# Optimization experiments

Measured on AMD Instinct MI355X. Metric: run time of the kernel, lower is better.

The kernel has to match this reference:

```python
import jax, jax.numpy as jnp
import numpy as np

KS_LIST = (7, 9, 11)
DILS = (1, 2, 4, 8, 16, 32)
PER = 5          # kernels per (kernel_size, dilation) group
EPS = 1e-5       # BatchNorm1d eps
N, C, L = 512, 12, 8192


def _rocket_features(x, W7, b7, W9, b9, W11, b11):
    # x: [N, C, L]; W_ks: [6*PER, C, ks]; b_ks: [6*PER]
    dn = ('NCH', 'OIH', 'NCH')
    feats = []
    for W, b in ((W7, b7), (W9, b9), (W11, b11)):
        for j, d in enumerate(DILS):
            w = W[j * PER:(j + 1) * PER]      # [PER, C, ks]
            bb = b[j * PER:(j + 1) * PER]     # [PER]
            # one dilated conv for all PER kernels in this group -> [N, PER, L]
            out = jax.lax.conv_general_dilated(
                x, w, window_strides=(1,), padding='SAME',
                rhs_dilation=(d,), dimension_numbers=dn) + bb[None, :, None]
            ppv = jnp.mean((out > 0).astype(x.dtype), axis=2)  # [N, PER]
            mx = jnp.max(out, axis=2)                          # [N, PER]
            # interleave (ppv_k, max_k) per kernel, matching the torch loop order
            feats.append(jnp.stack([ppv, mx], axis=-1).reshape(x.shape[0], 2 * PER))
    f = jnp.concatenate(feats, axis=1)  # [N, 2*nb_kernels] = [N, 180]
    # BatchNorm1d(affine=False), training mode: batch stats, biased variance
    mean = jnp.mean(f, axis=0)
    var = jnp.var(f, axis=0)
    return (f - mean) / jnp.sqrt(var + EPS)


def setup_inputs() -> dict:
    key = jax.random.key(0)
    kx, k1, k2, k3, k4, k5, k6 = jax.random.split(key, 7)
    G = len(DILS) * PER  # 30 kernels per kernel-size family
    inp = {
        'x': jax.random.normal(kx, (N, C, L), dtype=jnp.float32),
        'W7': jax.random.uniform(k1, (G, C, 7), minval=-1.0, maxval=1.0, dtype=jnp.float32),
        'b7': jax.random.normal(k2, (G,), dtype=jnp.float32),
        'W9': jax.random.uniform(k3, (G, C, 9), minval=-1.0, maxval=1.0, dtype=jnp.float32),
        'b9': jax.random.normal(k4, (G,), dtype=jnp.float32),
        'W11': jax.random.uniform(k5, (G, C, 11), minval=-1.0, maxval=1.0, dtype=jnp.float32),
        'b11': jax.random.normal(k6, (G,), dtype=jnp.float32),
    }
    return inp


def reference(x, W7, b7, W9, b9, W11, b11):
    return _rocket_features(x, W7, b7, W9, b9, W11, b11)
```

## Files before the change

### kernel.cpp

```cpp
#include <hip/hip_runtime.h>
#include <math.h>
#include <limits.h>

#define N_SAMP 512
#define C_IN   12
#define L_IN   8192
#define NDIL   6
#define NFILT  30
#define NFEAT  180
#define NCHUNK 4
#define CHUNK  (L_IN / NCHUNK)
#define EPSV   1e-5f

#define HALO   160
#define TLC    1024
#define LWC    (TLC + 2*HALO)
#define CELLS  (LWC + (LWC >> 4) + 1)
#define TILEB  (CELLS * 16)
#define NST    (CHUNK / TLC)

#define WF_OFF (3 * N_SAMP * NCHUNK * NFILT * 2)
#define WTAB_B (NDIL * 3 * 64 * 16)

typedef __attribute__((ext_vector_type(4))) int i32x4;

__device__ __forceinline__ int cellb(int r) {
    return (r + (r >> 4)) << 4;
}

__device__ __forceinline__ int imax(int a, int b) { return a > b ? a : b; }

__global__ __launch_bounds__(256)
void build_wb(const float* __restrict__ W7, const float* __restrict__ W9,
              const float* __restrict__ W11, const float* __restrict__ b7,
              const float* __restrict__ b9, const float* __restrict__ b11,
              signed char* __restrict__ wc, signed char* __restrict__ wd,
              float* __restrict__ bias_tab)
{
    const int t = blockIdx.x * 256 + threadIdx.x;
    if (t < NDIL * 3 * 64) {
        const int j    = t / 192;
        const int mf   = (t / 64) % 3;
        const int lane = t % 64;
        const int col  = lane & 15;
        const int q    = lane >> 4;
        const int tap  = mf * 4 + q;
#pragma unroll
        for (int e = 0; e < 16; ++e) {
            float v = 0.0f;
            if (col < 15 && tap <= 10 && e < 12) {
                const int toff = tap - 5;
                if (col < 5) {
                    if (toff >= -3 && toff <= 3)
                        v = W7[((j * 5 + col) * 12 + e) * 7 + toff + 3];
                } else if (col < 10) {
                    if (toff >= -4 && toff <= 4)
                        v = W9[((j * 5 + col - 5) * 12 + e) * 9 + toff + 4];
                } else {
                    v = W11[((j * 5 + col - 10) * 12 + e) * 11 + toff + 5];
                }
            }
            const int W  = __float2int_rn(v * 8192.0f);
            const int C8 = (W + 128) >> 8;
            const int D8 = W - (C8 << 8);
            wc[(size_t)t * 16 + e] = (signed char)C8;
            wd[(size_t)t * 16 + e] = (signed char)D8;
        }
    } else if (t < NDIL * 3 * 64 + 96) {
        const int i = t - NDIL * 3 * 64;
        const int j = i / 16, s = i % 16;
        float b = 0.0f;
        if (s < 5)       b = b7 [j * 5 + s];
        else if (s < 10) b = b9 [j * 5 + s - 5];
        else if (s < 15) b = b11[j * 5 + s - 10];
        bias_tab[j * 16 + s] = b;
    }
}

__global__ __launch_bounds__(256)
void rocket_conv_i8(const float* __restrict__ x,
                    const signed char* __restrict__ wc,
                    const signed char* __restrict__ wd,
                    const float* __restrict__ bias_tab,
                    float* __restrict__ ws)
{
    __shared__ __align__(16) signed char xq[2][TILEB];
    __shared__ int scnt[NDIL * 16];
    __shared__ int smx [NDIL * 16];

    const int ch  = blockIdx.x;
    const int n   = blockIdx.y;
    const int tid = threadIdx.x;
    const int lane = tid & 63, wv = tid >> 6;
    const int row_l = lane & 15, q = lane >> 4;
    const float* __restrict__ xrow = x + (size_t)n * C_IN * L_IN;
    const i32x4* __restrict__ wcv = (const i32x4*)wc;
    const i32x4* __restrict__ wdv = (const i32x4*)wd;

    if (tid < NDIL * 16) { scnt[tid] = 0; smx[tid] = INT_MIN; }

    const int c0 = ch * CHUNK;
#pragma unroll 1
    for (int st = 0; st < NST; ++st) {
        const int t0 = c0 + st * TLC;
        __syncthreads();
#pragma unroll 1
        for (int r = tid; r < LWC; r += 256) {
            const int g = t0 - HALO + r;
            int h[4] = {0, 0, 0, 0}, l[4] = {0, 0, 0, 0};
            if ((unsigned)g < (unsigned)L_IN) {
#pragma unroll
                for (int c = 0; c < 12; ++c) {
                    const float xv = xrow[c * L_IN + g];
                    const int X  = __float2int_rn(xv * 4096.0f);
                    const int A8 = (X + 128) >> 8;
                    const int B8 = X - (A8 << 8);
                    h[c >> 2] |= (A8 & 255) << ((c & 3) * 8);
                    l[c >> 2] |= (B8 & 255) << ((c & 3) * 8);
                }
            }
            const int cell = cellb(r);
            *(i32x4*)&xq[0][cell] = (i32x4){h[0], h[1], h[2], h[3]};
            *(i32x4*)&xq[1][cell] = (i32x4){l[0], l[1], l[2], l[3]};
        }
        __syncthreads();

#pragma unroll 1
        for (int j = 0; j < NDIL; ++j) {
            const int d = 1 << j;
            const i32x4 C0 = wcv[(j * 3 + 0) * 64 + lane];
            const i32x4 C1 = wcv[(j * 3 + 1) * 64 + lane];
            const i32x4 C2 = wcv[(j * 3 + 2) * 64 + lane];
            const i32x4 D0 = wdv[(j * 3 + 0) * 64 + lane];
            const i32x4 D1 = wdv[(j * 3 + 1) * 64 + lane];
            const i32x4 D2 = wdv[(j * 3 + 2) * 64 + lane];
            const float bj = bias_tab[j * 16 + row_l];
            const int tj = (int)floorf(bj * -33554432.0f);
            const int r0 = HALO + wv * 256 + row_l + (q - 5) * d;
            const int r1 = HALO + wv * 256 + row_l + (q - 1) * d;
            const int r2 = HALO + wv * 256 + row_l +
                           ((q == 3) ? 0 : (q + 3) * d);

            int cnt_i = 0, mx_i = INT_MIN;
#pragma unroll 4
            for (int t = 0; t < 16; ++t) {
                const int cell0 = cellb(r0 + 16 * t);
                const int cell1 = cellb(r1 + 16 * t);
                const int cell2 = cellb(r2 + 16 * t);
                i32x4 a0 = {0, 0, 0, 0};
                i32x4 a1 = {0, 0, 0, 0};
                i32x4 a2 = {0, 0, 0, 0};
                {
                    i32x4 ah = *(const i32x4*)&xq[0][cell0];
                    i32x4 al = *(const i32x4*)&xq[1][cell0];
                    a0 = __builtin_amdgcn_mfma_i32_16x16x64_i8(ah, C0, a0, 0, 0, 0);
                    a1 = __builtin_amdgcn_mfma_i32_16x16x64_i8(ah, D0, a1, 0, 0, 0);
                    a1 = __builtin_amdgcn_mfma_i32_16x16x64_i8(al, C0, a1, 0, 0, 0);
                    a2 = __builtin_amdgcn_mfma_i32_16x16x64_i8(al, D0, a2, 0, 0, 0);
                }
                {
                    i32x4 ah = *(const i32x4*)&xq[0][cell1];
                    i32x4 al = *(const i32x4*)&xq[1][cell1];
                    a0 = __builtin_amdgcn_mfma_i32_16x16x64_i8(ah, C1, a0, 0, 0, 0);
                    a1 = __builtin_amdgcn_mfma_i32_16x16x64_i8(ah, D1, a1, 0, 0, 0);
                    a1 = __builtin_amdgcn_mfma_i32_16x16x64_i8(al, C1, a1, 0, 0, 0);
                    a2 = __builtin_amdgcn_mfma_i32_16x16x64_i8(al, D1, a2, 0, 0, 0);
                }
                {
                    i32x4 ah = *(const i32x4*)&xq[0][cell2];
                    i32x4 al = *(const i32x4*)&xq[1][cell2];
                    a0 = __builtin_amdgcn_mfma_i32_16x16x64_i8(ah, C2, a0, 0, 0, 0);
                    a1 = __builtin_amdgcn_mfma_i32_16x16x64_i8(ah, D2, a1, 0, 0, 0);
                    a1 = __builtin_amdgcn_mfma_i32_16x16x64_i8(al, C2, a1, 0, 0, 0);
                    a2 = __builtin_amdgcn_mfma_i32_16x16x64_i8(al, D2, a2, 0, 0, 0);
                }
                const int v0 = ((a0[0] << 8) + a1[0] << 8) + a2[0];
                const int v1 = ((a0[1] << 8) + a1[1] << 8) + a2[1];
                const int v2 = ((a0[2] << 8) + a1[2] << 8) + a2[2];
                const int v3 = ((a0[3] << 8) + a1[3] << 8) + a2[3];
                cnt_i += (v0 > tj) + (v1 > tj) + (v2 > tj) + (v3 > tj);
                mx_i = imax(mx_i, imax(imax(v0, v1), imax(v2, v3)));
            }

            cnt_i += __shfl_xor(cnt_i, 16);
            cnt_i += __shfl_xor(cnt_i, 32);
            mx_i = imax(mx_i, __shfl_xor(mx_i, 16));
            mx_i = imax(mx_i, __shfl_xor(mx_i, 32));
            if (lane < 16) {
                atomicAdd(&scnt[j * 16 + lane], cnt_i);
                atomicMax(&smx[j * 16 + lane], mx_i);
            }
        }
    }

    __syncthreads();
    if (tid < 96) {
        const int jj = tid >> 4, s = tid & 15;
        if (s < 15) {
            const int c = scnt[jj * 16 + s];
            const int m = smx[jj * 16 + s];
            const float bj = bias_tab[jj * 16 + s];
            const int ks = s / 5, f = s % 5;
            const int gg = jj * 5 + f;
            const size_t base =
                ((((size_t)ks * N_SAMP + n) * NCHUNK + ch) * NFILT + gg) * 2;
            ws[base]     = (float)c;
            ws[base + 1] = bj + (float)m * 2.9802322387695312e-8f;
        }
    }
}

__global__ __launch_bounds__(512)
void rocket_finish(const float* __restrict__ ws, float* __restrict__ out)
{
    const int i = blockIdx.x;
    const int t = threadIdx.x;

    const int ks = i / 60;
    const int r  = i % 60;
    const int g  = r >> 1;
    const int m  = r & 1;

    const size_t base =
        ((((size_t)ks * N_SAMP + t) * NCHUNK) * NFILT + g) * 2 + m;

    float v;
    if (m) {
        v = -INFINITY;
#pragma unroll
        for (int c = 0; c < NCHUNK; ++c)
            v = fmaxf(v, ws[base + (size_t)c * NFILT * 2]);
    } else {
        v = 0.0f;
#pragma unroll
        for (int c = 0; c < NCHUNK; ++c)
            v += ws[base + (size_t)c * NFILT * 2];
        v *= (1.0f / (float)L_IN);
    }

    float s  = v;
    float sq = v * v;
#pragma unroll
    for (int off = 32; off; off >>= 1) {
        s  += __shfl_xor(s, off);
        sq += __shfl_xor(sq, off);
    }

    __shared__ float ss[8], sqq[8];
    const int lane = t & 63;
    const int wv   = t >> 6;
    if (lane == 0) { ss[wv] = s; sqq[wv] = sq; }
    __syncthreads();
    if (t == 0) {
        float S = 0.0f, Q = 0.0f;
#pragma unroll
        for (int w = 0; w < 8; ++w) { S += ss[w]; Q += sqq[w]; }
        ss[0] = S; sqq[0] = Q;
    }
    __syncthreads();

    const float mean = ss[0] * (1.0f / (float)N_SAMP);
    const float var  = sqq[0] * (1.0f / (float)N_SAMP) - mean * mean;
    out[t * NFEAT + i] = (v - mean) / sqrtf(var + EPSV);
}

extern "C" void kernel_launch(void* const* d_in, const int* in_sizes, int n_in,
                              void* d_out, int out_size, void* d_ws, size_t ws_size,
                              hipStream_t stream)
{
    const float* x   = (const float*)d_in[0];
    const float* W7  = (const float*)d_in[1];
    const float* b7  = (const float*)d_in[2];
    const float* W9  = (const float*)d_in[3];
    const float* b9  = (const float*)d_in[4];
    const float* W11 = (const float*)d_in[5];
    const float* b11 = (const float*)d_in[6];
    float* out = (float*)d_out;
    float* ws  = (float*)d_ws;
    signed char* wc = (signed char*)(ws + WF_OFF);
    signed char* wd = wc + WTAB_B;
    float* bias_tab = (float*)(wd + WTAB_B);

    build_wb<<<5, 256, 0, stream>>>(W7, W9, W11, b7, b9, b11, wc, wd, bias_tab);

    dim3 grid(NCHUNK, N_SAMP);
    rocket_conv_i8<<<grid, 256, 0, stream>>>(x, wc, wd, bias_tab, ws);

    rocket_finish<<<NFEAT, 512, 0, stream>>>(ws, out);
}
```

Before: 256.4 us.

## Reuse shared-memory A-fragments across tiles via sliding register windows for larger dilations

For dilations 4 through 32, the tap-to-lane mapping is rearranged so the rows read for successive 16-row tiles overlap. Each fragment loaded from LDS is then kept in registers and reused across iterations in a sliding window, instead of reloading three fragment pairs every tile. For dilations 16 and 32 the weight table uses a different tap ordering (3*q+mf), and the LDS tile is padded by 32 rows to hold the extra lookahead reads. The loops are fully unrolled, which raises register pressure and code size in return for fewer LDS loads.

Result: faster. 247.2 us (-3.6%).

```diff
diff --git a/kernel.cpp b/kernel.cpp
--- a/kernel.cpp
+++ b/kernel.cpp
@@ -15,7 +15,8 @@
 #define HALO   160
 #define TLC    1024
 #define LWC    (TLC + 2*HALO)
-#define CELLS  (LWC + (LWC >> 4) + 1)
+#define LWCP   (LWC + 32)
+#define CELLS  (LWCP + (LWCP >> 4) + 1)
 #define TILEB  (CELLS * 16)
 #define NST    (CHUNK / TLC)
 
@@ -29,6 +30,28 @@
 }
 
 __device__ __forceinline__ int imax(int a, int b) { return a > b ? a : b; }
+
+__device__ __forceinline__ void mfma_step(const i32x4 ah, const i32x4 al,
+                                          const i32x4 C, const i32x4 D,
+                                          i32x4& a0, i32x4& a1, i32x4& a2)
+{
+    a0 = __builtin_amdgcn_mfma_i32_16x16x64_i8(ah, C, a0, 0, 0, 0);
+    a1 = __builtin_amdgcn_mfma_i32_16x16x64_i8(ah, D, a1, 0, 0, 0);
+    a1 = __builtin_amdgcn_mfma_i32_16x16x64_i8(al, C, a1, 0, 0, 0);
+    a2 = __builtin_amdgcn_mfma_i32_16x16x64_i8(al, D, a2, 0, 0, 0);
+}
+
+__device__ __forceinline__ void tile_stats(const i32x4 a0, const i32x4 a1,
+                                           const i32x4 a2, int tj,
+                                           int& cnt_i, int& mx_i)
+{
+    const int v0 = (((a0[0] << 8) + a1[0]) << 8) + a2[0];
+    const int v1 = (((a0[1] << 8) + a1[1]) << 8) + a2[1];
+    const int v2 = (((a0[2] << 8) + a1[2]) << 8) + a2[2];
+    const int v3 = (((a0[3] << 8) + a1[3]) << 8) + a2[3];
+    cnt_i += (v0 > tj) + (v1 > tj) + (v2 > tj) + (v3 > tj);
+    mx_i = imax(mx_i, imax(imax(v0, v1), imax(v2, v3)));
+}
 
 __global__ __launch_bounds__(256)
 void build_wb(const float* __restrict__ W7, const float* __restrict__ W9,
@@ -44,7 +67,7 @@
         const int lane = t % 64;
         const int col  = lane & 15;
         const int q    = lane >> 4;
-        const int tap  = mf * 4 + q;
+        const int tap  = (j >= 4) ? (3 * q + mf) : (mf * 4 + q);
 #pragma unroll
         for (int e = 0; e < 16; ++e) {
             float v = 0.0f;
@@ -99,6 +122,75 @@
 
     if (tid < NDIL * 16) { scnt[tid] = 0; smx[tid] = INT_MIN; }
 
+#define RDH(ROW) (*(const i32x4*)&xq[0][cellb(ROW)])
+#define RDL(ROW) (*(const i32x4*)&xq[1][cellb(ROW)])
+
+    auto flush = [&](int j, int cnt_i, int mx_i) {
+        cnt_i += __shfl_xor(cnt_i, 16);
+        cnt_i += __shfl_xor(cnt_i, 32);
+        mx_i = imax(mx_i, __shfl_xor(mx_i, 16));
+        mx_i = imax(mx_i, __shfl_xor(mx_i, 32));
+        if (lane < 16) {
+            atomicAdd(&scnt[j * 16 + lane], cnt_i);
+            atomicMax(&smx[j * 16 + lane], mx_i);
+        }
+    };
+
+    auto win3 = [&](int j, int lane_off) {
+        const i32x4 C0 = wcv[(j * 3 + 0) * 64 + lane];
+        const i32x4 C1 = wcv[(j * 3 + 1) * 64 + lane];
+        const i32x4 C2 = wcv[(j * 3 + 2) * 64 + lane];
+        const i32x4 D0 = wdv[(j * 3 + 0) * 64 + lane];
+        const i32x4 D1 = wdv[(j * 3 + 1) * 64 + lane];
+        const i32x4 D2 = wdv[(j * 3 + 2) * 64 + lane];
+        const int tj = (int)floorf(bias_tab[j * 16 + row_l] * -33554432.0f);
+        const int rb = HALO + wv * 256 + row_l + lane_off;
+        i32x4 h0 = RDH(rb),      l0 = RDL(rb);
+        i32x4 h1 = RDH(rb + 16), l1 = RDL(rb + 16);
+        int cnt_i = 0, mx_i = INT_MIN;
+#pragma unroll
+        for (int t = 0; t < 16; ++t) {
+            i32x4 h2 = RDH(rb + 16 * (t + 2));
+            i32x4 l2 = RDL(rb + 16 * (t + 2));
+            i32x4 a0 = {0,0,0,0}, a1 = {0,0,0,0}, a2 = {0,0,0,0};
+            mfma_step(h0, l0, C0, D0, a0, a1, a2);
+            mfma_step(h1, l1, C1, D1, a0, a1, a2);
+            mfma_step(h2, l2, C2, D2, a0, a1, a2);
+            tile_stats(a0, a1, a2, tj, cnt_i, mx_i);
+            h0 = h1; l0 = l1; h1 = h2; l1 = l2;
+        }
+        flush(j, cnt_i, mx_i);
+    };
+
+    auto win5 = [&](int j, int lane_off) {
+        const i32x4 C0 = wcv[(j * 3 + 0) * 64 + lane];
+        const i32x4 C1 = wcv[(j * 3 + 1) * 64 + lane];
+        const i32x4 C2 = wcv[(j * 3 + 2) * 64 + lane];
+        const i32x4 D0 = wdv[(j * 3 + 0) * 64 + lane];
+        const i32x4 D1 = wdv[(j * 3 + 1) * 64 + lane];
+        const i32x4 D2 = wdv[(j * 3 + 2) * 64 + lane];
+        const int tj = (int)floorf(bias_tab[j * 16 + row_l] * -33554432.0f);
+        const int rb = HALO + wv * 256 + row_l + lane_off;
+        i32x4 h0 = RDH(rb),      l0 = RDL(rb);
+        i32x4 h1 = RDH(rb + 16), l1 = RDL(rb + 16);
+        i32x4 h2 = RDH(rb + 32), l2 = RDL(rb + 32);
+        i32x4 h3 = RDH(rb + 48), l3 = RDL(rb + 48);
+        int cnt_i = 0, mx_i = INT_MIN;
+#pragma unroll
+        for (int t = 0; t < 16; ++t) {
+            i32x4 h4 = RDH(rb + 16 * (t + 4));
+            i32x4 l4 = RDL(rb + 16 * (t + 4));
+            i32x4 a0 = {0,0,0,0}, a1 = {0,0,0,0}, a2 = {0,0,0,0};
+            mfma_step(h0, l0, C0, D0, a0, a1, a2);
+            mfma_step(h2, l2, C1, D1, a0, a1, a2);
+            mfma_step(h4, l4, C2, D2, a0, a1, a2);
+            tile_stats(a0, a1, a2, tj, cnt_i, mx_i);
+            h0 = h1; l0 = l1; h1 = h2; l1 = l2;
+            h2 = h3; l2 = l3; h3 = h4; l3 = l4;
+        }
+        flush(j, cnt_i, mx_i);
+    };
+
     const int c0 = ch * CHUNK;
 #pragma unroll 1
     for (int st = 0; st < NST; ++st) {
@@ -126,7 +218,7 @@
         __syncthreads();
 
 #pragma unroll 1
-        for (int j = 0; j < NDIL; ++j) {
+        for (int j = 0; j < 2; ++j) {
             const int d = 1 << j;
             const i32x4 C0 = wcv[(j * 3 + 0) * 64 + lane];
             const i32x4 C1 = wcv[(j * 3 + 1) * 64 + lane];
@@ -134,63 +226,30 @@
             const i32x4 D0 = wdv[(j * 3 + 0) * 64 + lane];
             const i32x4 D1 = wdv[(j * 3 + 1) * 64 + lane];
             const i32x4 D2 = wdv[(j * 3 + 2) * 64 + lane];
-            const float bj = bias_tab[j * 16 + row_l];
-            const int tj = (int)floorf(bj * -33554432.0f);
-            const int r0 = HALO + wv * 256 + row_l + (q - 5) * d;
-            const int r1 = HALO + wv * 256 + row_l + (q - 1) * d;
-            const int r2 = HALO + wv * 256 + row_l +
-                           ((q == 3) ? 0 : (q + 3) * d);
-
+            const int tj = (int)floorf(bias_tab[j * 16 + row_l] * -33554432.0f);
+            const int rb0 = HALO + wv * 256 + row_l + (q - 5) * d;
+            const int rb1 = rb0 + 4 * d;
+            const int rb2 = rb0 + 8 * d;
             int cnt_i = 0, mx_i = INT_MIN;
 #pragma unroll 4
             for (int t = 0; t < 16; ++t) {
-                const int cell0 = cellb(r0 + 16 * t);
-                const int cell1 = cellb(r1 + 16 * t);
-                const int cell2 = cellb(r2 + 16 * t);
-                i32x4 a0 = {0, 0, 0, 0};
-                i32x4 a1 = {0, 0, 0, 0};
-                i32x4 a2 = {0, 0, 0, 0};
-                {
-                    i32x4 ah = *(const i32x4*)&xq[0][cell0];
-                    i32x4 al = *(const i32x4*)&xq[1][cell0];
-                    a0 = __builtin_amdgcn_mfma_i32_16x16x64_i8(ah, C0, a0, 0, 0, 0);
-                    a1 = __builtin_amdgcn_mfma_i32_16x16x64_i8(ah, D0, a1, 0, 0, 0);
-                    a1 = __builtin_amdgcn_mfma_i32_16x16x64_i8(al, C0, a1, 0, 0, 0);
-                    a2 = __builtin_amdgcn_mfma_i32_16x16x64_i8(al, D0, a2, 0, 0, 0);
-                }
-                {
-                    i32x4 ah = *(const i32x4*)&xq[0][cell1];
-                    i32x4 al = *(const i32x4*)&xq[1][cell1];
-                    a0 = __builtin_amdgcn_mfma_i32_16x16x64_i8(ah, C1, a0, 0, 0, 0);
-                    a1 = __builtin_amdgcn_mfma_i32_16x16x64_i8(ah, D1, a1, 0, 0, 0);
-                    a1 = __builtin_amdgcn_mfma_i32_16x16x64_i8(al, C1, a1, 0, 0, 0);
-                    a2 = __builtin_amdgcn_mfma_i32_16x16x64_i8(al, D1, a2, 0, 0, 0);
-                }
-                {
-                    i32x4 ah = *(const i32x4*)&xq[0][cell2];
-                    i32x4 al = *(const i32x4*)&xq[1][cell2];
-                    a0 = __builtin_amdgcn_mfma_i32_16x16x64_i8(ah, C2, a0, 0, 0, 0);
-                    a1 = __builtin_amdgcn_mfma_i32_16x16x64_i8(ah, D2, a1, 0, 0, 0);
-                    a1 = __builtin_amdgcn_mfma_i32_16x16x64_i8(al, C2, a1, 0, 0, 0);
-                    a2 = __builtin_amdgcn_mfma_i32_16x16x64_i8(al, D2, a2, 0, 0, 0);
-                }
-                const int v0 = ((a0[0] << 8) + a1[0] << 8) + a2[0];
-                const int v1 = ((a0[1] << 8) + a1[1] << 8) + a2[1];
-                const int v2 = ((a0[2] << 8) + a1[2] << 8) + a2[2];
-                const int v3 = ((a0[3] << 8) + a1[3] << 8) + a2[3];
-                cnt_i += (v0 > tj) + (v1 > tj) + (v2 > tj) + (v3 > tj);
-                mx_i = imax(mx_i, imax(imax(v0, v1), imax(v2, v3)));
+                const int o = 16 * t;
+                i32x4 ah0 = RDH(rb0 + o), al0 = RDL(rb0 + o);
+                i32x4 ah1 = RDH(rb1 + o), al1 = RDL(rb1 + o);
+                i32x4 ah2 = RDH(rb2 + o), al2 = RDL(rb2 + o);
+                i32x4 a0 = {0,0,0,0}, a1 = {0,0,0,0}, a2 = {0,0,0,0};
+                mfma_step(ah0, al0, C0, D0, a0, a1, a2);
+                mfma_step(ah1, al1, C1, D1, a0, a1, a2);
+                mfma_step(ah2, al2, C2, D2, a0, a1, a2);
+                tile_stats(a0, a1, a2, tj, cnt_i, mx_i);
             }
-
-            cnt_i += __shfl_xor(cnt_i, 16);
-            cnt_i += __shfl_xor(cnt_i, 32);
-            mx_i = imax(mx_i, __shfl_xor(mx_i, 16));
-            mx_i = imax(mx_i, __shfl_xor(mx_i, 32));
-            if (lane < 16) {
-                atomicAdd(&scnt[j * 16 + lane], cnt_i);
-                atomicMax(&smx[j * 16 + lane], mx_i);
-            }
-        }
+            flush(j, cnt_i, mx_i);
+        }
+
+        win3(2, (q - 5) * 4);
+        win5(3, (q - 5) * 8);
+        win3(4, (3 * q - 5) * 16);
+        win5(5, (3 * q - 5) * 32);
     }
 
     __syncthreads();
@@ -208,6 +267,8 @@
             ws[base + 1] = bj + (float)m * 2.9802322387695312e-8f;
         }
     }
+#undef RDH
+#undef RDL
 }
 
 __global__ __launch_bounds__(512)
```
